# Kernel optimization log

Hardware: AMD Instinct MI355X
Metric: run time of the kernel (lower is better)

## Reference

```python
import jax, jax.numpy as jnp
import numpy as np

B, T, N, D = 8, 128, 256, 64  # batch, timesteps, nodes, d_model
LN_EPS = 1e-5


def _ln(x, g, b):
    m = x.mean(-1, keepdims=True)
    v = ((x - m) ** 2).mean(-1, keepdims=True)
    return (x - m) / jnp.sqrt(v + LN_EPS) * g + b


def setup_inputs() -> dict:
    key = jax.random.key(0)
    ks = jax.random.split(key, 12)
    s = 0.05
    f32 = jnp.float32
    return {
        "H_i": jax.random.normal(ks[0], (B, T, N, D), dtype=f32),
        "H_j": jax.random.normal(ks[1], (B, T, N, D), dtype=f32),
        # CrossModalTemporalAligner params (torch Linear: y = x @ W.T + b, W is [out,in])
        "Wq": jax.random.normal(ks[2], (D, D), dtype=f32) * s, "bq": jnp.zeros((D,), f32),
        "Wk": jax.random.normal(ks[3], (D, D), dtype=f32) * s, "bk": jnp.zeros((D,), f32),
        "Wv": jax.random.normal(ks[4], (D, D), dtype=f32) * s, "bv": jnp.zeros((D,), f32),
        "log_gamma": jnp.zeros((), f32),
        "log_tau": jnp.zeros((), f32),
        # GCNMambaLayer params
        "e1": jax.random.normal(ks[5], (N, 32), dtype=f32),
        "e2": jax.random.normal(ks[6], (32, N), dtype=f32),
        "Wg": jax.random.normal(ks[7], (D, D), dtype=f32) * s, "bg": jnp.zeros((D,), f32),
        "ln1_g": jnp.ones((D,), f32), "ln1_b": jnp.zeros((D,), f32),
        # GRU fallback for Mamba block (torch nn.GRU: gates order r,z,n)
        "Wih": jax.random.normal(ks[8], (3 * D, D), dtype=f32) * s,
        "Whh": jax.random.normal(ks[9], (3 * D, D), dtype=f32) * s,
        "bih": jnp.zeros((3 * D,), f32), "bhh": jnp.zeros((3 * D,), f32),
        "ln2_g": jnp.ones((D,), f32), "ln2_b": jnp.zeros((D,), f32),
    }


def _aligner(H_i, H_j, Wq, bq, Wk, bk, Wv, bv, log_gamma, log_tau):
    b, Ti, n, d = H_i.shape
    Tj = H_j.shape[1]
    Q = jnp.einsum("btnd,ed->btne", H_i, Wq) + bq
    K = jnp.einsum("btnd,ed->btne", H_j, Wk) + bk
    V = jnp.einsum("btnd,ed->btne", H_j, Wv) + bv
    # per-node temporal attention: [B, N, Ti, Tj]
    tau = jnp.clip(jnp.exp(log_tau), 0.01)
    sim = jnp.einsum("bind,bjnd->bnij", Q, K) / (d ** 0.5 * tau)
    t_i = jnp.arange(Ti, dtype=jnp.float32) / max(Ti - 1, 1)
    t_j = jnp.arange(Tj, dtype=jnp.float32) / max(Tj - 1, 1)
    gamma = jnp.clip(jnp.exp(log_gamma), 0.01)
    decay = jnp.exp(-gamma * jnp.abs(t_i[:, None] - t_j[None, :]))  # [Ti, Tj]
    sim = sim + jnp.log(decay + 1e-8)[None, None]
    attn = jax.nn.softmax(sim, axis=-1)
    out = jnp.einsum("bnij,bjnd->bind", attn, V)  # back to [B, Ti, N, d]
    return out


def _gru(x_tn, Wih, Whh, bih, bhh):
    # x_tn: [B, N, T, d]; scan over T, carry h: [B, N, d]
    d = x_tn.shape[-1]
    xs = jnp.moveaxis(x_tn, 2, 0)  # [T, B, N, d]
    h0 = jnp.zeros(x_tn.shape[:2] + (d,), x_tn.dtype)

    def step(h, x_t):
        gi = x_t @ Wih.T + bih
        gh = h @ Whh.T + bhh
        i_r, i_z, i_n = jnp.split(gi, 3, axis=-1)
        h_r, h_z, h_n = jnp.split(gh, 3, axis=-1)
        r = jax.nn.sigmoid(i_r + h_r)
        z = jax.nn.sigmoid(i_z + h_z)
        n = jnp.tanh(i_n + r * h_n)
        h_new = (1.0 - z) * n + z * h
        return h_new, h_new

    _, outs = jax.lax.scan(step, h0, xs)
    return jnp.moveaxis(outs, 0, 2)  # [B, N, T, d]


def _gcn_mamba(x, e1, e2, Wg, bg, ln1_g, ln1_b, Wih, Whh, bih, bhh, ln2_g, ln2_b):
    # adaptive adjacency: softmax over dim=1 (columns) of relu(e1@e2)
    adp = jax.nn.softmax(jax.nn.relu(e1 @ e2), axis=1)  # [N, N]
    h_gcn = jax.nn.relu(jnp.einsum("mn,btnd->btmd", adp, x) @ Wg.T + bg)
    x = _ln(x + h_gcn, ln1_g, ln1_b)  # dropout is identity in eval
    x_tn = jnp.transpose(x, (0, 2, 1, 3))  # [B, N, T, d]
    ssm_out = _gru(x_tn, Wih, Whh, bih, bhh)
    h_mb = _ln(x_tn + ssm_out, ln2_g, ln2_b)  # MambaTemporalBlock: norm(x + ssm(x))
    x = x + jnp.transpose(h_mb, (0, 2, 1, 3))
    return x


def reference(H_i, H_j, Wq, bq, Wk, bk, Wv, bv, log_gamma, log_tau,
              e1, e2, Wg, bg, ln1_g, ln1_b, Wih, Whh, bih, bhh, ln2_g, ln2_b):
    aligned = _aligner(H_i, H_j, Wq, bq, Wk, bk, Wv, bv, log_gamma, log_tau)
    return _gcn_mamba(aligned, e1, e2, Wg, bg, ln1_g, ln1_b,
                      Wih, Whh, bih, bhh, ln2_g, ln2_b)
```

## Files before the change

kernel.cpp:

```cpp
#include <hip/hip_runtime.h>
#include <cstddef>

#define BB 8
#define TT 128
#define NN 256
#define DD 64

typedef _Float16 half2_t __attribute__((ext_vector_type(2)));
typedef _Float16 half4_t __attribute__((ext_vector_type(4)));
typedef _Float16 half8_t __attribute__((ext_vector_type(8)));
typedef float f32x4 __attribute__((ext_vector_type(4)));

#if defined(__has_builtin)
#  if __has_builtin(__builtin_amdgcn_fdot2)
#    define FDOT2(a,b,c) __builtin_amdgcn_fdot2((a),(b),(c),false)
#  endif
#endif
#ifndef FDOT2
#  define FDOT2(a,b,c) ((c) + (float)(a).x*(float)(b).x + (float)(a).y*(float)(b).y)
#endif

union h8u { half8_t v; half2_t h[4]; };

__global__ __launch_bounds__(256) void k_prep(
    const float* __restrict__ Wq, const float* __restrict__ Wk, const float* __restrict__ Wv,
    const float* __restrict__ Wg,
    unsigned int* __restrict__ wq2, unsigned int* __restrict__ wk2,
    unsigned int* __restrict__ wv2, unsigned int* __restrict__ wg2)
{
  int t = blockIdx.x * 256 + threadIdx.x;
  if (t < 2048) {
    half2_t a; a.x = (_Float16)Wq[2*t]; a.y = (_Float16)Wq[2*t+1];
    wq2[t] = __builtin_bit_cast(unsigned int, a);
    half2_t b; b.x = (_Float16)Wk[2*t]; b.y = (_Float16)Wk[2*t+1];
    wk2[t] = __builtin_bit_cast(unsigned int, b);
    half2_t c; c.x = (_Float16)Wv[2*t]; c.y = (_Float16)Wv[2*t+1];
    wv2[t] = __builtin_bit_cast(unsigned int, c);
    half2_t d; d.x = (_Float16)Wg[2*t]; d.y = (_Float16)Wg[2*t+1];
    wg2[t] = __builtin_bit_cast(unsigned int, d);
  }
}

#define KSTR 72
#define PSTR 136

__device__ __forceinline__ half8_t wfrag(const unsigned int* __restrict__ W2, int e, int k0) {
  return *(const half8_t*)(W2 + e * 32 + (k0 >> 1));
}

__global__ __launch_bounds__(256, 2) void k_attn(
    const float* __restrict__ Hi, const float* __restrict__ Hj,
    const unsigned int* __restrict__ wq2, const unsigned int* __restrict__ wk2,
    const unsigned int* __restrict__ wv2,
    const float* __restrict__ bq, const float* __restrict__ bk, const float* __restrict__ bv,
    const float* __restrict__ lgp, const float* __restrict__ ltp,
    float* __restrict__ out)
{
  __shared__ __align__(16) _Float16 sK[TT][KSTR];
  __shared__ __align__(16) _Float16 sVt[DD][PSTR];
  __shared__ __align__(16) _Float16 sP[4][32][PSTR];
  __shared__ float sDecay[TT];

  const int b   = blockIdx.x >> 8;
  const int n   = blockIdx.x & 255;
  const int tid = threadIdx.x;
  const int w   = tid >> 6;
  const int l   = tid & 63;
  const int l16 = l & 15;
  const int lg4 = l >> 4;

  const float gamma = fmaxf(__expf(lgp[0]), 0.01f);
  const float tau   = fmaxf(__expf(ltp[0]), 0.01f);
  const float scale = 1.0f / (8.0f * tau);
  if (tid < TT) {
    float dt = gamma * (float)tid * (1.0f / 127.0f);
    sDecay[tid] = __logf(__expf(-dt) + 1e-8f);
  }

  const int row0 = 32 * w;
  half8_t hai[2][2], haj[2][2];
  #pragma unroll
  for (int mt = 0; mt < 2; mt++) {
    const int i = row0 + 16 * mt + l16;
    const float* ri = Hi + (((size_t)b * TT + i) * NN + n) * DD;
    const float* rj = Hj + (((size_t)b * TT + i) * NN + n) * DD;
    #pragma unroll
    for (int ks = 0; ks < 2; ks++) {
      const int k0 = 32 * ks + 8 * lg4;
      float4 a = *(const float4*)(ri + k0);
      float4 c = *(const float4*)(ri + k0 + 4);
      half8_t h;
      h[0]=(_Float16)a.x; h[1]=(_Float16)a.y; h[2]=(_Float16)a.z; h[3]=(_Float16)a.w;
      h[4]=(_Float16)c.x; h[5]=(_Float16)c.y; h[6]=(_Float16)c.z; h[7]=(_Float16)c.w;
      hai[mt][ks] = h;
      a = *(const float4*)(rj + k0);
      c = *(const float4*)(rj + k0 + 4);
      h[0]=(_Float16)a.x; h[1]=(_Float16)a.y; h[2]=(_Float16)a.z; h[3]=(_Float16)a.w;
      h[4]=(_Float16)c.x; h[5]=(_Float16)c.y; h[6]=(_Float16)c.z; h[7]=(_Float16)c.w;
      haj[mt][ks] = h;
    }
  }

  #pragma unroll
  for (int nt = 0; nt < 4; nt++) {
    const int e = 16 * nt + l16;
    half8_t wb0 = wfrag(wq2, e, 8 * lg4);
    half8_t wb1 = wfrag(wq2, e, 32 + 8 * lg4);
    const float be = bq[e];
    #pragma unroll
    for (int mt = 0; mt < 2; mt++) {
      f32x4 acc = {be, be, be, be};
      acc = __builtin_amdgcn_mfma_f32_16x16x32_f16(hai[mt][0], wb0, acc, 0, 0, 0);
      acc = __builtin_amdgcn_mfma_f32_16x16x32_f16(hai[mt][1], wb1, acc, 0, 0, 0);
      #pragma unroll
      for (int r = 0; r < 4; r++)
        sP[w][16 * mt + 4 * lg4 + r][e] = (_Float16)(acc[r] * scale);
    }
  }

  #pragma unroll
  for (int nt = 0; nt < 4; nt++) {
    const int e = 16 * nt + l16;
    half8_t wb0 = wfrag(wk2, e, 8 * lg4);
    half8_t wb1 = wfrag(wk2, e, 32 + 8 * lg4);
    const float be = bk[e];
    #pragma unroll
    for (int mt = 0; mt < 2; mt++) {
      f32x4 acc = {be, be, be, be};
      acc = __builtin_amdgcn_mfma_f32_16x16x32_f16(haj[mt][0], wb0, acc, 0, 0, 0);
      acc = __builtin_amdgcn_mfma_f32_16x16x32_f16(haj[mt][1], wb1, acc, 0, 0, 0);
      #pragma unroll
      for (int r = 0; r < 4; r++)
        sK[row0 + 16 * mt + 4 * lg4 + r][e] = (_Float16)acc[r];
    }
  }

  #pragma unroll
  for (int nt = 0; nt < 4; nt++) {
    const int e = 16 * nt + l16;
    half8_t wb0 = wfrag(wv2, e, 8 * lg4);
    half8_t wb1 = wfrag(wv2, e, 32 + 8 * lg4);
    const float be = bv[e];
    #pragma unroll
    for (int mt = 0; mt < 2; mt++) {
      f32x4 acc = {be, be, be, be};
      acc = __builtin_amdgcn_mfma_f32_16x16x32_f16(haj[mt][0], wb0, acc, 0, 0, 0);
      acc = __builtin_amdgcn_mfma_f32_16x16x32_f16(haj[mt][1], wb1, acc, 0, 0, 0);
      const int jb = row0 + 16 * mt + 4 * lg4;
      half4_t v4;
      v4[0] = (_Float16)acc[0]; v4[1] = (_Float16)acc[1];
      v4[2] = (_Float16)acc[2]; v4[3] = (_Float16)acc[3];
      *(half4_t*)(&sVt[e][jb]) = v4;
    }
  }
  __syncthreads();

  half8_t qa[2][2];
  #pragma unroll
  for (int mt = 0; mt < 2; mt++)
    #pragma unroll
    for (int ks = 0; ks < 2; ks++)
      qa[mt][ks] = *(const half8_t*)(&sP[w][16 * mt + l16][32 * ks + 8 * lg4]);

  float rs[2][4] = {{0.f,0.f,0.f,0.f},{0.f,0.f,0.f,0.f}};
  for (int jt = 0; jt < 8; jt++) {
    const int j = 16 * jt + l16;
    half8_t kb0 = *(const half8_t*)(&sK[j][8 * lg4]);
    half8_t kb1 = *(const half8_t*)(&sK[j][32 + 8 * lg4]);
    #pragma unroll
    for (int mt = 0; mt < 2; mt++) {
      f32x4 acc = {0.f, 0.f, 0.f, 0.f};
      acc = __builtin_amdgcn_mfma_f32_16x16x32_f16(qa[mt][0], kb0, acc, 0, 0, 0);
      acc = __builtin_amdgcn_mfma_f32_16x16x32_f16(qa[mt][1], kb1, acc, 0, 0, 0);
      #pragma unroll
      for (int r = 0; r < 4; r++) {
        const int il = 16 * mt + 4 * lg4 + r;
        int di = (row0 + il) - j; di = di < 0 ? -di : di;
        float p = __expf(acc[r] + sDecay[di]);
        rs[mt][r] += p;
        sP[w][il][j] = (_Float16)p;
      }
    }
  }

  f32x4 oacc[2][4] = {};
  #pragma unroll
  for (int ks = 0; ks < 4; ks++) {
    const int j0 = 32 * ks + 8 * lg4;
    half8_t pa0 = *(const half8_t*)(&sP[w][l16][j0]);
    half8_t pa1 = *(const half8_t*)(&sP[w][16 + l16][j0]);
    #pragma unroll
    for (int nt = 0; nt < 4; nt++) {
      half8_t vb = *(const half8_t*)(&sVt[16 * nt + l16][j0]);
      oacc[0][nt] = __builtin_amdgcn_mfma_f32_16x16x32_f16(pa0, vb, oacc[0][nt], 0, 0, 0);
      oacc[1][nt] = __builtin_amdgcn_mfma_f32_16x16x32_f16(pa1, vb, oacc[1][nt], 0, 0, 0);
    }
  }

  #pragma unroll
  for (int mt = 0; mt < 2; mt++)
    #pragma unroll
    for (int r = 0; r < 4; r++) {
      float v = rs[mt][r];
      v += __shfl_xor(v, 1, 64);
      v += __shfl_xor(v, 2, 64);
      v += __shfl_xor(v, 4, 64);
      v += __shfl_xor(v, 8, 64);
      rs[mt][r] = 1.0f / v;
    }
  #pragma unroll
  for (int mt = 0; mt < 2; mt++) {
    #pragma unroll
    for (int r = 0; r < 4; r++) {
      const int i = row0 + 16 * mt + 4 * lg4 + r;
      float* orow = out + (((size_t)b * TT + i) * NN + n) * DD;
      const float rl = rs[mt][r];
      #pragma unroll
      for (int nt = 0; nt < 4; nt++)
        orow[16 * nt + l16] = oacc[mt][nt][r] * rl;
    }
  }
}

__global__ __launch_bounds__(256) void k_adp(
    const float* __restrict__ e1, const float* __restrict__ e2,
    unsigned short* __restrict__ adph)
{
  const int m = blockIdx.x, n = threadIdx.x;
  float s = 0.f;
  #pragma unroll
  for (int k = 0; k < 32; k++) s += e1[m*32+k] * e2[k*256+n];
  s = fmaxf(s, 0.f);
  __shared__ float red[256];
  red[n] = s; __syncthreads();
  for (int off = 128; off > 0; off >>= 1) {
    if (n < off) red[n] = fmaxf(red[n], red[n+off]);
    __syncthreads();
  }
  float mx = red[0];
  __syncthreads();
  float p = __expf(s - mx);
  red[n] = p; __syncthreads();
  for (int off = 128; off > 0; off >>= 1) {
    if (n < off) red[n] += red[n+off];
    __syncthreads();
  }
  _Float16 h = (_Float16)(p / red[0]);
  adph[m*256 + n] = __builtin_bit_cast(unsigned short, h);
}

#define GSTR 280

__global__ __launch_bounds__(256, 2) void k_gcn(
    float* __restrict__ x, const unsigned short* __restrict__ adph,
    const unsigned int* __restrict__ wg2, const float* __restrict__ bg,
    const float* __restrict__ g1, const float* __restrict__ b1)
{
  __shared__ __align__(16) _Float16 sxhT[DD][GSTR];
  __shared__ __align__(16) _Float16 sgT[DD][GSTR];

  const int tid = threadIdx.x;
  const int w   = tid >> 6;
  const int l   = tid & 63;
  const int l16 = l & 15;
  const int lg4 = l >> 4;
  float* tile = x + (size_t)blockIdx.x * NN * DD;

  {
    const int d2 = tid & 31;
    const int mg = tid >> 5;
    #pragma unroll
    for (int it = 0; it < 16; it++) {
      const int m0 = mg * 2 + it * 16;
      float2 va = *(const float2*)(tile + (size_t)m0 * DD + 2 * d2);
      float2 vb = *(const float2*)(tile + (size_t)(m0 + 1) * DD + 2 * d2);
      half2_t h0; h0.x = (_Float16)va.x; h0.y = (_Float16)vb.x;
      half2_t h1; h1.x = (_Float16)va.y; h1.y = (_Float16)vb.y;
      *(half2_t*)(&sxhT[2 * d2][m0])     = h0;
      *(half2_t*)(&sxhT[2 * d2 + 1][m0]) = h1;
    }
  }
  __syncthreads();

  f32x4 acc1[4][4] = {};
  for (int ks = 0; ks < 8; ks++) {
    const int k0 = 32 * ks + 8 * lg4;
    half8_t bfr[4], afr[4];
    #pragma unroll
    for (int nt = 0; nt < 4; nt++)
      bfr[nt] = *(const half8_t*)(&sxhT[16 * nt + l16][k0]);
    #pragma unroll
    for (int mt = 0; mt < 4; mt++) {
      const int m = 64 * w + 16 * mt + l16;
      afr[mt] = *(const half8_t*)(adph + m * 256 + k0);
    }
    #pragma unroll
    for (int mt = 0; mt < 4; mt++)
      #pragma unroll
      for (int nt = 0; nt < 4; nt++)
        acc1[mt][nt] = __builtin_amdgcn_mfma_f32_16x16x32_f16(afr[mt], bfr[nt], acc1[mt][nt], 0, 0, 0);
  }

  #pragma unroll
  for (int mt = 0; mt < 4; mt++)
    #pragma unroll
    for (int nt = 0; nt < 4; nt++) {
      half4_t g4;
      g4[0] = (_Float16)acc1[mt][nt][0]; g4[1] = (_Float16)acc1[mt][nt][1];
      g4[2] = (_Float16)acc1[mt][nt][2]; g4[3] = (_Float16)acc1[mt][nt][3];
      *(half4_t*)(&sgT[16 * nt + l16][64 * w + 16 * mt + 4 * lg4]) = g4;
    }
  __syncthreads();

  half8_t wb[4][2];
  float bgv[4], g1v[4], b1v[4];
  #pragma unroll
  for (int et = 0; et < 4; et++) {
    const int e = 16 * et + l16;
    wb[et][0] = wfrag(wg2, e, 8 * lg4);
    wb[et][1] = wfrag(wg2, e, 32 + 8 * lg4);
    bgv[et] = bg[e]; g1v[et] = g1[e]; b1v[et] = b1[e];
  }

  #pragma unroll 1
  for (int mt = 0; mt < 4; mt++) {
    half8_t ga[2];
    #pragma unroll
    for (int ks = 0; ks < 2; ks++) {
      half8_t h;
      #pragma unroll
      for (int j = 0; j < 8; j++)
        h[j] = sgT[32 * ks + 8 * lg4 + j][64 * w + 16 * mt + l16];
      ga[ks] = h;
    }
    f32x4 acc2[4];
    #pragma unroll
    for (int et = 0; et < 4; et++) {
      f32x4 a = {bgv[et], bgv[et], bgv[et], bgv[et]};
      a = __builtin_amdgcn_mfma_f32_16x16x32_f16(ga[0], wb[et][0], a, 0, 0, 0);
      a = __builtin_amdgcn_mfma_f32_16x16x32_f16(ga[1], wb[et][1], a, 0, 0, 0);
      acc2[et] = a;
    }
    #pragma unroll
    for (int r = 0; r < 4; r++) {
      const int mrow = 64 * w + 16 * mt + 4 * lg4 + r;
      float* xr = tile + (size_t)mrow * DD;
      float y[4], s1 = 0.f, s2 = 0.f;
      #pragma unroll
      for (int et = 0; et < 4; et++) {
        float h = fmaxf(acc2[et][r], 0.f);
        float yv = xr[16 * et + l16] + h;
        y[et] = yv; s1 += yv; s2 += yv * yv;
      }
      #pragma unroll
      for (int off = 1; off < 16; off <<= 1) {
        s1 += __shfl_xor(s1, off, 64);
        s2 += __shfl_xor(s2, off, 64);
      }
      const float mean = s1 * (1.f / 64.f);
      const float var  = fmaxf(s2 * (1.f / 64.f) - mean * mean, 0.f);
      const float rstd = rsqrtf(var + 1e-5f);
      #pragma unroll
      for (int et = 0; et < 4; et++)
        xr[16 * et + l16] = (y[et] - mean) * rstd * g1v[et] + b1v[et];
    }
  }
}

__global__ __launch_bounds__(256) void k_gih(
    const float* __restrict__ x, const float* __restrict__ Wih,
    const float* __restrict__ bih, unsigned int* __restrict__ GI2)
{
  __shared__ unsigned int sW[192*32];
  __shared__ unsigned int sbuf[256*33];
  const int tid = threadIdx.x;
  const int b = blockIdx.x >> 7, t = blockIdx.x & 127;
  const float* xt = x + (((size_t)b * TT + t) * NN) * DD;

  for (int idx = tid; idx < 192*32; idx += 256) {
    float2 w = ((const float2*)Wih)[idx];
    half2_t h; h.x = (_Float16)w.x; h.y = (_Float16)w.y;
    sW[idx] = __builtin_bit_cast(unsigned int, h);
  }
  for (int idx = tid; idx < 256*32; idx += 256) {
    int n = idx >> 5, k = idx & 31;
    float2 v = ((const float2*)xt)[idx];
    half2_t h; h.x = (_Float16)v.x; h.y = (_Float16)v.y;
    sbuf[n*33 + k] = __builtin_bit_cast(unsigned int, h);
  }
  __syncthreads();
  half2_t xr[32];
  #pragma unroll
  for (int k = 0; k < 32; k++) xr[k] = __builtin_bit_cast(half2_t, sbuf[tid*33 + k]);
  __syncthreads();

  const size_t blockbase = ((size_t)t * 2048 + b * 256) * 96;
  for (int c = 0; c < 4; c++) {
    #pragma unroll 2
    for (int j2 = 0; j2 < 24; j2++) {
      int e0 = c*48 + 2*j2;
      float a0 = bih[e0], a1 = bih[e0+1];
      const half8_t* w0 = (const half8_t*)(sW + e0*32);
      const half8_t* w1 = (const half8_t*)(sW + (e0+1)*32);
      #pragma unroll
      for (int kq = 0; kq < 8; kq++) {
        h8u ua, ub; ua.v = w0[kq]; ub.v = w1[kq];
        #pragma unroll
        for (int m = 0; m < 4; m++) {
          a0 = FDOT2(ua.h[m], xr[4*kq+m], a0);
          a1 = FDOT2(ub.h[m], xr[4*kq+m], a1);
        }
      }
      half2_t o; o.x = (_Float16)a0; o.y = (_Float16)a1;
      sbuf[tid*25 + j2] = __builtin_bit_cast(unsigned int, o);
    }
    __syncthreads();
    for (int idx = tid; idx < 6144; idx += 256) {
      int n = idx / 24, e2 = idx % 24;
      GI2[blockbase + (size_t)n*96 + c*24 + e2] = sbuf[n*25 + e2];
    }
    __syncthreads();
  }
}

__global__ __launch_bounds__(256) void k_gru_gi(
    float* __restrict__ x, const _Float16* __restrict__ GIh,
    const float* __restrict__ Whh, const float* __restrict__ bhh,
    const float* __restrict__ g2, const float* __restrict__ b2)
{
  __shared__ __align__(16) _Float16 hsh[4*64];
  __shared__ float ghs[4*192];
  const int tid = threadIdx.x;
  const int b = blockIdx.x >> 6, n4 = blockIdx.x & 63;
  const int s = tid >> 6, d = tid & 63;

  half2_t wh[32];
  float bh = 0.f;
  if (tid < 192) {
    bh = bhh[tid];
    const float2* wr = (const float2*)Whh;
    #pragma unroll
    for (int k = 0; k < 32; k++) {
      float2 w = wr[tid*32 + k];
      half2_t h; h.x = (_Float16)w.x; h.y = (_Float16)w.y;
      wh[k] = h;
    }
  }
  hsh[tid] = (_Float16)0.f;
  const float lng = g2[d], lnb = b2[d];
  float hreg = 0.f;
  size_t gioff = ((size_t)b*256 + n4*4 + s)*192 + d;
  size_t xoff  = (((size_t)b * TT) * NN + n4*4 + s)*DD + d;
  __syncthreads();

  for (int t = 0; t < TT; t++) {
    float gir = (float)GIh[gioff];
    float giz = (float)GIh[gioff + 64];
    float gin = (float)GIh[gioff + 128];
    float xv  = x[xoff];

    if (tid < 192) {
      float a0 = bh, a1 = bh, a2 = bh, a3 = bh;
      const half8_t* h8 = (const half8_t*)hsh;
      #pragma unroll
      for (int kq = 0; kq < 8; kq++) {
        h8u u0, u1, u2, u3;
        u0.v = h8[kq]; u1.v = h8[8+kq]; u2.v = h8[16+kq]; u3.v = h8[24+kq];
        #pragma unroll
        for (int m = 0; m < 4; m++) {
          half2_t w = wh[4*kq + m];
          a0 = FDOT2(w, u0.h[m], a0);
          a1 = FDOT2(w, u1.h[m], a1);
          a2 = FDOT2(w, u2.h[m], a2);
          a3 = FDOT2(w, u3.h[m], a3);
        }
      }
      ghs[tid] = a0; ghs[192 + tid] = a1; ghs[384 + tid] = a2; ghs[576 + tid] = a3;
    }
    __syncthreads();

    float rr = gir + ghs[s*192 + d];
    float zz = giz + ghs[s*192 + 64 + d];
    float hn_ = ghs[s*192 + 128 + d];
    float r = 1.f / (1.f + __expf(-rr));
    float z = 1.f / (1.f + __expf(-zz));
    float e = __expf(2.f * (gin + r * hn_));
    float nt = 1.f - 2.f / (e + 1.f);
    float hn = (1.f - z) * nt + z * hreg;
    hreg = hn;

    float yv = xv + hn;
    float s1 = yv, s2v = yv * yv;
    #pragma unroll
    for (int off = 32; off > 0; off >>= 1) {
      s1  += __shfl_xor(s1,  off, 64);
      s2v += __shfl_xor(s2v, off, 64);
    }
    float mean = s1 * 0.015625f;
    float var  = fmaxf(s2v * 0.015625f - mean * mean, 0.f);
    float hm = (yv - mean) * rsqrtf(var + 1e-5f) * lng + lnb;

    x[xoff] = xv + hm;
    hsh[tid] = (_Float16)hn;
    __syncthreads();

    gioff += (size_t)2048 * 192;
    xoff  += (size_t)NN * DD;
  }
}

__global__ __launch_bounds__(256) void k_gru(
    float* __restrict__ x,
    const float* __restrict__ Wih, const float* __restrict__ Whh,
    const float* __restrict__ bih, const float* __restrict__ bhh,
    const float* __restrict__ g2, const float* __restrict__ b2)
{
  __shared__ half2_t sWi[192][33];
  __shared__ half2_t sWh[192][33];
  __shared__ float   xs[4][64];
  __shared__ half2_t xs_h[4][32];
  __shared__ float   hs_f[4][64];
  __shared__ half2_t hs_h[4][32];
  __shared__ float   gis[4][192];
  __shared__ float   ghs[4][192];

  const int b  = blockIdx.x >> 6;
  const int ng = blockIdx.x & 63;

  for (int idx = threadIdx.x; idx < 192 * 32; idx += 256) {
    int g = idx >> 5, dh = idx & 31;
    half2_t hv; hv.x = (_Float16)Wih[g*64 + 2*dh]; hv.y = (_Float16)Wih[g*64 + 2*dh + 1];
    sWi[g][dh] = hv;
    half2_t hw; hw.x = (_Float16)Whh[g*64 + 2*dh]; hw.y = (_Float16)Whh[g*64 + 2*dh + 1];
    sWh[g][dh] = hw;
  }
  const int s_d = threadIdx.x >> 6;
  const int d_d = threadIdx.x & 63;
  hs_f[s_d][d_d] = 0.f;
  ((_Float16*)hs_h[s_d])[d_d] = (_Float16)0.f;
  const float lng = g2[d_d], lnb = b2[d_d];

  int   tsk_s[3], tsk_g[3];
  float tb_i[3], tb_h[3];
  #pragma unroll
  for (int k = 0; k < 3; k++) {
    int task = threadIdx.x + k * 256;
    tsk_s[k] = task / 192; tsk_g[k] = task % 192;
    tb_i[k] = bih[tsk_g[k]]; tb_h[k] = bhh[tsk_g[k]];
  }
  __syncthreads();

  const size_t base = (((size_t)b * TT) * NN + ng * 4) * DD;
  for (int t = 0; t < TT; t++) {
    const size_t row = base + (size_t)t * NN * DD + s_d * 64 + d_d;
    float xv = x[row];
    xs[s_d][d_d] = xv;
    ((_Float16*)xs_h[s_d])[d_d] = (_Float16)xv;
    __syncthreads();

    #pragma unroll
    for (int k = 0; k < 3; k++) {
      int s = tsk_s[k], g = tsk_g[k];
      float ai = tb_i[k], ah = tb_h[k];
      #pragma unroll
      for (int dh = 0; dh < 32; dh++) {
        ai = FDOT2(sWi[g][dh], xs_h[s][dh], ai);
        ah = FDOT2(sWh[g][dh], hs_h[s][dh], ah);
      }
      gis[s][g] = ai; ghs[s][g] = ah;
    }
    __syncthreads();

    float gr = gis[s_d][d_d]      + ghs[s_d][d_d];
    float gz = gis[s_d][64 + d_d] + ghs[s_d][64 + d_d];
    float r  = 1.f / (1.f + __expf(-gr));
    float z  = 1.f / (1.f + __expf(-gz));
    float nn = tanhf(gis[s_d][128 + d_d] + r * ghs[s_d][128 + d_d]);
    float ho = hs_f[s_d][d_d];
    float hn = (1.f - z) * nn + z * ho;

    float yv = xs[s_d][d_d] + hn;
    float s1 = yv, s2 = yv * yv;
    #pragma unroll
    for (int off = 32; off > 0; off >>= 1) {
      s1 += __shfl_xor(s1, off, 64);
      s2 += __shfl_xor(s2, off, 64);
    }
    float mean = s1 * (1.f / 64.f);
    float var  = fmaxf(s2 * (1.f / 64.f) - mean * mean, 0.f);
    float hm = (yv - mean) * rsqrtf(var + 1e-5f) * lng + lnb;

    x[row] = xs[s_d][d_d] + hm;
    hs_f[s_d][d_d] = hn;
    ((_Float16*)hs_h[s_d])[d_d] = (_Float16)hn;
    __syncthreads();
  }
}

extern "C" void kernel_launch(void* const* d_in, const int* in_sizes, int n_in,
                              void* d_out, int out_size, void* d_ws, size_t ws_size,
                              hipStream_t stream) {
  const float* Hi  = (const float*)d_in[0];
  const float* Hj  = (const float*)d_in[1];
  const float* Wq  = (const float*)d_in[2];  const float* bq = (const float*)d_in[3];
  const float* Wk  = (const float*)d_in[4];  const float* bk = (const float*)d_in[5];
  const float* Wv  = (const float*)d_in[6];  const float* bv = (const float*)d_in[7];
  const float* lg  = (const float*)d_in[8];  const float* lt = (const float*)d_in[9];
  const float* e1  = (const float*)d_in[10]; const float* e2 = (const float*)d_in[11];
  const float* Wg  = (const float*)d_in[12]; const float* bg = (const float*)d_in[13];
  const float* g1  = (const float*)d_in[14]; const float* b1 = (const float*)d_in[15];
  const float* Wih = (const float*)d_in[16]; const float* Whh = (const float*)d_in[17];
  const float* bih = (const float*)d_in[18]; const float* bhh = (const float*)d_in[19];
  const float* g2  = (const float*)d_in[20]; const float* b2  = (const float*)d_in[21];
  float* out  = (float*)d_out;

  unsigned short* adph = (unsigned short*)d_ws;
  unsigned int* wg2 = (unsigned int*)d_ws + 32768;
  unsigned int* wq2 = (unsigned int*)d_ws + 65536;
  unsigned int* wk2 = wq2 + 2048;
  unsigned int* wv2 = wk2 + 2048;
  const size_t gi_off = 286720;
  const size_t gi_bytes = (size_t)2048 * TT * 192 * 2;
  const bool use_gi = ws_size >= gi_off + gi_bytes;
  unsigned int* GI2 = (unsigned int*)((char*)d_ws + gi_off);
  _Float16*     GIh = (_Float16*)((char*)d_ws + gi_off);

  k_prep<<<dim3(8),     dim3(256), 0, stream>>>(Wq, Wk, Wv, Wg, wq2, wk2, wv2, wg2);
  k_attn<<<dim3(BB*NN), dim3(256), 0, stream>>>(Hi, Hj, wq2, wk2, wv2, bq, bk, bv, lg, lt, out);
  k_adp <<<dim3(NN),    dim3(256), 0, stream>>>(e1, e2, adph);
  k_gcn <<<dim3(BB*TT), dim3(256), 0, stream>>>(out, adph, wg2, bg, g1, b1);
  if (use_gi) {
    k_gih   <<<dim3(BB*TT), dim3(256), 0, stream>>>(out, Wih, bih, GI2);
    k_gru_gi<<<dim3(512),   dim3(256), 0, stream>>>(out, GIh, Whh, bhh, g2, b2);
  } else {
    k_gru   <<<dim3(512),   dim3(256), 0, stream>>>(out, Wih, Whh, bih, bhh, g2, b2);
  }
}
```

Baseline: 559.1 us.

## Make GRU recurrence wave-local with readlane broadcast and prefetch next step

The GRU recurrence kernel now gives each wavefront one node and has each lane compute the r, z and n hidden-gate dot products for its own feature. The hidden state is broadcast with readlane from a packed half2 register instead of going through shared memory. This removes both block-wide barriers and the shared-memory round trips on every timestep. The next timestep's gate inputs and x values are prefetched to hide global load latency. The cost is three times as many weight registers per lane (96 half2) plus a launch-bounds occupancy hint, which raises register pressure.

```diff
diff --git a/kernel.cpp b/kernel.cpp
--- a/kernel.cpp
+++ b/kernel.cpp
@@ -423,89 +423,91 @@
   }
 }
 
-__global__ __launch_bounds__(256) void k_gru_gi(
+__global__ __launch_bounds__(256, 2) void k_gru_gi(
     float* __restrict__ x, const _Float16* __restrict__ GIh,
     const float* __restrict__ Whh, const float* __restrict__ bhh,
     const float* __restrict__ g2, const float* __restrict__ b2)
 {
-  __shared__ __align__(16) _Float16 hsh[4*64];
-  __shared__ float ghs[4*192];
   const int tid = threadIdx.x;
+  const int w = tid >> 6;
+  const int l = tid & 63;
   const int b = blockIdx.x >> 6, n4 = blockIdx.x & 63;
-  const int s = tid >> 6, d = tid & 63;
-
-  half2_t wh[32];
-  float bh = 0.f;
-  if (tid < 192) {
-    bh = bhh[tid];
-    const float2* wr = (const float2*)Whh;
+
+  half2_t wr[32], wz[32], wn[32];
+  {
+    const float2* Wr = (const float2*)(Whh + (size_t)l * 64);
+    const float2* Wz = (const float2*)(Whh + (size_t)(64 + l) * 64);
+    const float2* Wn = (const float2*)(Whh + (size_t)(128 + l) * 64);
     #pragma unroll
     for (int k = 0; k < 32; k++) {
-      float2 w = wr[tid*32 + k];
-      half2_t h; h.x = (_Float16)w.x; h.y = (_Float16)w.y;
-      wh[k] = h;
-    }
-  }
-  hsh[tid] = (_Float16)0.f;
-  const float lng = g2[d], lnb = b2[d];
+      float2 a = Wr[k]; half2_t ha; ha.x = (_Float16)a.x; ha.y = (_Float16)a.y; wr[k] = ha;
+      float2 c = Wz[k]; half2_t hc; hc.x = (_Float16)c.x; hc.y = (_Float16)c.y; wz[k] = hc;
+      float2 e = Wn[k]; half2_t he; he.x = (_Float16)e.x; he.y = (_Float16)e.y; wn[k] = he;
+    }
+  }
+  const float bhr = bhh[l], bhz = bhh[64 + l], bhn = bhh[128 + l];
+  const float lng = g2[l], lnb = b2[l];
+
   float hreg = 0.f;
-  size_t gioff = ((size_t)b*256 + n4*4 + s)*192 + d;
-  size_t xoff  = (((size_t)b * TT) * NN + n4*4 + s)*DD + d;
-  __syncthreads();
+  unsigned int h2pack = 0;
+
+  const size_t gistride = (size_t)2048 * 192;
+  const size_t xstride  = (size_t)NN * DD;
+  size_t gioff = ((size_t)b * 256 + n4 * 4 + w) * 192 + l;
+  size_t xoff  = (((size_t)b * TT) * NN + n4 * 4 + w) * DD + l;
+
+  float gir = (float)GIh[gioff];
+  float giz = (float)GIh[gioff + 64];
+  float gin = (float)GIh[gioff + 128];
+  float xv  = x[xoff];
+
+  const int li = l & 31;
 
   for (int t = 0; t < TT; t++) {
-    float gir = (float)GIh[gioff];
-    float giz = (float)GIh[gioff + 64];
-    float gin = (float)GIh[gioff + 128];
-    float xv  = x[xoff];
-
-    if (tid < 192) {
-      float a0 = bh, a1 = bh, a2 = bh, a3 = bh;
-      const half8_t* h8 = (const half8_t*)hsh;
-      #pragma unroll
-      for (int kq = 0; kq < 8; kq++) {
-        h8u u0, u1, u2, u3;
-        u0.v = h8[kq]; u1.v = h8[8+kq]; u2.v = h8[16+kq]; u3.v = h8[24+kq];
-        #pragma unroll
-        for (int m = 0; m < 4; m++) {
-          half2_t w = wh[4*kq + m];
-          a0 = FDOT2(w, u0.h[m], a0);
-          a1 = FDOT2(w, u1.h[m], a1);
-          a2 = FDOT2(w, u2.h[m], a2);
-          a3 = FDOT2(w, u3.h[m], a3);
-        }
-      }
-      ghs[tid] = a0; ghs[192 + tid] = a1; ghs[384 + tid] = a2; ghs[576 + tid] = a3;
-    }
-    __syncthreads();
-
-    float rr = gir + ghs[s*192 + d];
-    float zz = giz + ghs[s*192 + 64 + d];
-    float hn_ = ghs[s*192 + 128 + d];
-    float r = 1.f / (1.f + __expf(-rr));
-    float z = 1.f / (1.f + __expf(-zz));
-    float e = __expf(2.f * (gin + r * hn_));
-    float nt = 1.f - 2.f / (e + 1.f);
-    float hn = (1.f - z) * nt + z * hreg;
+    const size_t adv = (t + 1 < TT) ? 1 : 0;
+    const size_t gioff_n = gioff + adv * gistride;
+    const size_t xoff_n  = xoff  + adv * xstride;
+    float gir_n = (float)GIh[gioff_n];
+    float giz_n = (float)GIh[gioff_n + 64];
+    float gin_n = (float)GIh[gioff_n + 128];
+    float xv_n  = x[xoff_n];
+
+    float ar = bhr, az = bhz, an = bhn;
+    #pragma unroll
+    for (int k = 0; k < 32; k++) {
+      half2_t s2 = __builtin_bit_cast(half2_t,
+                     __builtin_amdgcn_readlane((int)h2pack, k));
+      ar = FDOT2(wr[k], s2, ar);
+      az = FDOT2(wz[k], s2, az);
+      an = FDOT2(wn[k], s2, an);
+    }
+
+    const float r = 1.f / (1.f + __expf(-(gir + ar)));
+    const float z = 1.f / (1.f + __expf(-(giz + az)));
+    const float e = __expf(2.f * (gin + r * an));
+    const float nt = 1.f - 2.f / (e + 1.f);
+    const float hn = (1.f - z) * nt + z * hreg;
     hreg = hn;
 
-    float yv = xv + hn;
+    const float yv = xv + hn;
     float s1 = yv, s2v = yv * yv;
     #pragma unroll
     for (int off = 32; off > 0; off >>= 1) {
       s1  += __shfl_xor(s1,  off, 64);
       s2v += __shfl_xor(s2v, off, 64);
     }
-    float mean = s1 * 0.015625f;
-    float var  = fmaxf(s2v * 0.015625f - mean * mean, 0.f);
-    float hm = (yv - mean) * rsqrtf(var + 1e-5f) * lng + lnb;
-
+    const float mean = s1 * 0.015625f;
+    const float var  = fmaxf(s2v * 0.015625f - mean * mean, 0.f);
+    const float hm = (yv - mean) * rsqrtf(var + 1e-5f) * lng + lnb;
     x[xoff] = xv + hm;
-    hsh[tid] = (_Float16)hn;
-    __syncthreads();
-
-    gioff += (size_t)2048 * 192;
-    xoff  += (size_t)NN * DD;
+
+    const float hae = __shfl(hn, 2 * li, 64);
+    const float hbe = __shfl(hn, 2 * li + 1, 64);
+    half2_t hp; hp.x = (_Float16)hae; hp.y = (_Float16)hbe;
+    h2pack = __builtin_bit_cast(unsigned int, hp);
+
+    gir = gir_n; giz = giz_n; gin = gin_n; xv = xv_n;
+    gioff += gistride; xoff += xstride;
   }
 }
 
```

Result: no change. 550.0 us (-1.6%).
